# Kernel optimization log

Measured on AMD Instinct MI355X. Metric: run time of the kernel, lower is better.

## Reference

```python
import jax, jax.numpy as jnp
import numpy as np

SAMPLE_RATE = 4096.0  # matches init_kwargs sample_rate
STATE_DIM = 64
LENGTH, CHANNELS = 8192, 512


def setup_inputs() -> dict:
    key = jax.random.key(0)
    kx, kc = jax.random.split(key)
    x = jax.random.normal(kx, (LENGTH, CHANNELS), dtype=jnp.float32)
    # param init exactly as in the flax module
    logA = jnp.log(1.0 + jnp.arange(STATE_DIM, dtype=jnp.float32))
    B = jnp.ones((STATE_DIM,), dtype=jnp.float32)
    C = 0.01 * jax.random.normal(kc, (STATE_DIM,), dtype=jnp.float32)  # nn.initializers.normal() stddev=0.01
    return {"x": x, "logA": logA, "B": B, "C": C}


def reference(x, logA, B, C):
    # ZOH-style discretization: A = -exp(logA); Abar = exp(A*dt); Bbar = (Abar-1)*B/A
    dt = 1.0 / SAMPLE_RATE
    A = -jnp.exp(logA)                # (N,)
    Abar = jnp.exp(A * dt)            # (N,)
    Bbar = (Abar - 1.0) * B / A       # (N,)

    channels = x.shape[1]
    h0 = jnp.zeros((channels, logA.shape[0]), dtype=x.dtype)  # (C, N)

    def step(h, xt):
        # h: (C, N), xt: (C,)
        h = Abar[None, :] * h + xt[:, None] * Bbar[None, :]
        y = h @ C                      # (C,)
        return h, y

    _, y = jax.lax.scan(step, h0, x)   # y: (L, C)
    return y
```

## Files before the change

kernel.cpp:

```cpp
#include <hip/hip_runtime.h>
#include <math.h>

#define LENGTH   8192
#define CHANNELS 512
#define NSTATE   64
#define TCHUNK   64
#define NCHUNK   (LENGTH / TCHUNK)
#define E_ELEMS  (NCHUNK * NSTATE * CHANNELS)


__global__ void k_setup(const float* __restrict__ logA, const float* __restrict__ B,
                        const float* __restrict__ C, float* __restrict__ cons,
                        float* __restrict__ Gt, float* __restrict__ Tt,
                        float* __restrict__ Pt) {
    __shared__ double contrib[64][65];
    __shared__ double Kd[64];
    int n = threadIdx.x;

    double A    = -exp((double)logA[n]);
    double ab   = exp(A * (1.0 / 4096.0));
    double Bbar = (ab - 1.0) * (double)B[n] / A;
    double CB   = (double)C[n] * Bbar;

    cons[n]       = (float)ab;
    cons[64 + n]  = (float)CB;
    cons[128 + n] = (float)exp(A * (64.0 / 4096.0));

    double p = 1.0;
    #pragma unroll 1
    for (int e = 0; e < 64; ++e) { Gt[(63 - e) * 64 + n] = (float)p; p *= ab; }

    p = ab;
    #pragma unroll 1
    for (int t = 0; t < 64; ++t) { Pt[n * 64 + t] = (float)(CB * p); p *= ab; }

    p = CB;
    #pragma unroll 1
    for (int d = 0; d < 64; ++d) { contrib[n][d] = p; p *= ab; }
    __syncthreads();

    double Ksum = 0.0;
    #pragma unroll 1
    for (int m = 0; m < 64; ++m) Ksum += contrib[m][n];
    Kd[n] = Ksum;
    __syncthreads();

    int s = n;
    #pragma unroll 1
    for (int t = 0; t < 64; ++t) Tt[s * 64 + t] = (t >= s) ? (float)Kd[t - s] : 0.f;
}

__global__ __launch_bounds__(256, 4) void k_pass1(const float* __restrict__ x,
                                                  const float* __restrict__ Gt,
                                                  float* __restrict__ E) {
    __shared__ float Xl[64 * 64];
    int tid = threadIdx.x;
    int k   = blockIdx.x >> 3;
    int c0  = (blockIdx.x & 7) * 64;

    const float* xsrc = x + (size_t)k * TCHUNK * CHANNELS + c0;
    #pragma unroll
    for (int i = 0; i < 4; ++i) {
        int idx = tid + 256 * i;
        int s   = idx >> 4;
        int cq  = (idx & 15) * 4;
        *(float4*)&Xl[s * 64 + cq] = *(const float4*)(xsrc + (size_t)s * CHANNELS + cq);
    }
    __syncthreads();

    int w    = __builtin_amdgcn_readfirstlane(tid >> 6);
    int lane = tid & 63;
    const float* Gw = Gt + 16 * w;

    float acc[16];
    #pragma unroll
    for (int j = 0; j < 16; ++j) acc[j] = 0.f;

    #pragma unroll 4
    for (int s = 0; s < 64; ++s) {
        float xv = Xl[s * 64 + lane];
        const float* g = Gw + s * 64;
        #pragma unroll
        for (int j = 0; j < 16; ++j) acc[j] = fmaf(g[j], xv, acc[j]);
    }

    float* Ep = E + ((size_t)k * NSTATE + 16 * w) * CHANNELS + c0 + lane;
    #pragma unroll
    for (int j = 0; j < 16; ++j) Ep[(size_t)j * CHANNELS] = acc[j];
}

#define G2 16
__global__ __launch_bounds__(64, 1) void k_pass2(float* __restrict__ W,
                                                 const float* __restrict__ cons) {
    int gtid = blockIdx.x * 64 + threadIdx.x;
    int c = gtid & (CHANNELS - 1);
    int n = gtid >> 9;
    float aT = cons[128 + n];
    float* p = W + (size_t)n * CHANNELS + c;
    const size_t S = (size_t)NSTATE * CHANNELS;

    float e[2][G2];
    #pragma unroll
    for (int j = 0; j < G2; ++j) e[0][j] = p[(size_t)j * S];

    float hc = 0.f;
    #pragma unroll
    for (int k0 = 0; k0 < NCHUNK; k0 += G2) {
        const int cur = (k0 / G2) & 1;
        const int nxt = cur ^ 1;
        if (k0 + G2 < NCHUNK) {
            #pragma unroll
            for (int j = 0; j < G2; ++j) e[nxt][j] = p[(size_t)(k0 + G2 + j) * S];
        }
        #pragma unroll
        for (int j = 0; j < G2; ++j) {
            p[(size_t)(k0 + j) * S] = hc;
            hc = fmaf(aT, hc, e[cur][j]);
        }
    }
}

__global__ __launch_bounds__(256, 4) void k_pass3(const float* __restrict__ x,
                                                  const float* __restrict__ Tt,
                                                  const float* __restrict__ Pt,
                                                  const float* __restrict__ Wc,
                                                  float* __restrict__ y) {
    __shared__ float Xl[64 * 64];
    __shared__ float Hl[64 * 64];
    int tid = threadIdx.x;
    int k   = blockIdx.x >> 3;
    int c0  = (blockIdx.x & 7) * 64;

    const float* xsrc = x  + (size_t)k * TCHUNK * CHANNELS + c0;
    const float* hsrc = Wc + (size_t)k * NSTATE * CHANNELS + c0;
    #pragma unroll
    for (int i = 0; i < 4; ++i) {
        int idx = tid + 256 * i;
        int s   = idx >> 4;
        int cq  = (idx & 15) * 4;
        *(float4*)&Xl[s * 64 + cq] = *(const float4*)(xsrc + (size_t)s * CHANNELS + cq);
        *(float4*)&Hl[s * 64 + cq] = *(const float4*)(hsrc + (size_t)s * CHANNELS + cq);
    }
    __syncthreads();

    int w    = __builtin_amdgcn_readfirstlane(tid >> 6);
    int lane = tid & 63;
    int t0   = 16 * w;

    float acc[16];
    #pragma unroll
    for (int j = 0; j < 16; ++j) acc[j] = 0.f;

    const float* Tw = Tt + t0;
    #pragma unroll 4
    for (int s = 0; s < 64; ++s) {
        float xv = Xl[s * 64 + lane];
        const float* tt = Tw + s * 64;
        #pragma unroll
        for (int j = 0; j < 16; ++j) acc[j] = fmaf(tt[j], xv, acc[j]);
    }

    const float* Pw = Pt + t0;
    #pragma unroll 4
    for (int n = 0; n < 64; ++n) {
        float hv = Hl[n * 64 + lane];
        const float* pp = Pw + n * 64;
        #pragma unroll
        for (int j = 0; j < 16; ++j) acc[j] = fmaf(pp[j], hv, acc[j]);
    }

    float* yp = y + ((size_t)k * TCHUNK + t0) * CHANNELS + c0 + lane;
    #pragma unroll
    for (int j = 0; j < 16; ++j) yp[(size_t)j * CHANNELS] = acc[j];
}

__global__ __launch_bounds__(256) void k_fallback(const float* __restrict__ x,
                                                  const float* __restrict__ logA,
                                                  const float* __restrict__ B,
                                                  const float* __restrict__ C,
                                                  float* __restrict__ y) {
    int c = blockIdx.x * blockDim.x + threadIdx.x;
    if (c >= CHANNELS) return;
    float Abar[NSTATE], CB[NSTATE], h[NSTATE];
    for (int n = 0; n < NSTATE; ++n) {
        double A    = -exp((double)logA[n]);
        double ab   = exp(A * (1.0 / 4096.0));
        double Bbar = (ab - 1.0) * (double)B[n] / A;
        Abar[n] = (float)ab;
        CB[n]   = (float)((double)C[n] * Bbar);
        h[n]    = 0.f;
    }
    for (int t = 0; t < LENGTH; ++t) {
        float xv = x[(size_t)t * CHANNELS + c];
        float acc = 0.f;
        for (int n = 0; n < NSTATE; ++n) {
            h[n] = fmaf(Abar[n], h[n], xv);
            acc  = fmaf(CB[n], h[n], acc);
        }
        y[(size_t)t * CHANNELS + c] = acc;
    }
}

extern "C" void kernel_launch(void* const* d_in, const int* in_sizes, int n_in,
                              void* d_out, int out_size, void* d_ws, size_t ws_size,
                              hipStream_t stream) {
    const float* x    = (const float*)d_in[0];
    const float* logA = (const float*)d_in[1];
    const float* B    = (const float*)d_in[2];
    const float* C    = (const float*)d_in[3];
    float* yout = (float*)d_out;

    size_t need = (size_t)(E_ELEMS + 192 + 3 * 4096) * sizeof(float);
    if (ws_size < need) {
        k_fallback<<<(CHANNELS + 255) / 256, 256, 0, stream>>>(x, logA, B, C, yout);
        return;
    }

    float* W    = (float*)d_ws;
    float* cons = W + E_ELEMS;
    float* Gt   = cons + 192;
    float* Tt   = Gt + 4096;
    float* Pt   = Tt + 4096;

    k_setup<<<1, 64, 0, stream>>>(logA, B, C, cons, Gt, Tt, Pt);
    k_pass1<<<NCHUNK * 8, 256, 0, stream>>>(x, Gt, W);
    k_pass2<<<(NSTATE * CHANNELS) / 64, 64, 0, stream>>>(W, cons);
    k_pass3<<<NCHUNK * 8, 256, 0, stream>>>(x, Tt, Pt, W, yout);
}
```

Baseline: 113.9 us.

## Fold setup kernel into passes and use 4x4 register-tiled LDS matmuls

Removes the single-block double-precision setup kernel and instead recomputes the decay powers, Toeplitz kernel and output projection tables in shared memory inside each pass block using fp32 exp2f. The inner products in pass1 and pass3 change from per-lane scalar loops reading tables from global memory to a 4x4 register tile that reads float4 operands from LDS. This removes one serial launch and its double-precision latency, at the cost of redundant per-block table construction, more LDS use (lower occupancy bound in pass3) and reduced precision in the coefficients.

```diff
diff --git a/kernel.cpp b/kernel.cpp
--- a/kernel.cpp
+++ b/kernel.cpp
@@ -7,95 +7,74 @@
 #define TCHUNK   64
 #define NCHUNK   (LENGTH / TCHUNK)
 #define E_ELEMS  (NCHUNK * NSTATE * CHANNELS)
-
-
-__global__ void k_setup(const float* __restrict__ logA, const float* __restrict__ B,
-                        const float* __restrict__ C, float* __restrict__ cons,
-                        float* __restrict__ Gt, float* __restrict__ Tt,
-                        float* __restrict__ Pt) {
-    __shared__ double contrib[64][65];
-    __shared__ double Kd[64];
-    int n = threadIdx.x;
-
-    double A    = -exp((double)logA[n]);
-    double ab   = exp(A * (1.0 / 4096.0));
-    double Bbar = (ab - 1.0) * (double)B[n] / A;
-    double CB   = (double)C[n] * Bbar;
-
-    cons[n]       = (float)ab;
-    cons[64 + n]  = (float)CB;
-    cons[128 + n] = (float)exp(A * (64.0 / 4096.0));
-
-    double p = 1.0;
-    #pragma unroll 1
-    for (int e = 0; e < 64; ++e) { Gt[(63 - e) * 64 + n] = (float)p; p *= ab; }
-
-    p = ab;
-    #pragma unroll 1
-    for (int t = 0; t < 64; ++t) { Pt[n * 64 + t] = (float)(CB * p); p *= ab; }
-
-    p = CB;
-    #pragma unroll 1
-    for (int d = 0; d < 64; ++d) { contrib[n][d] = p; p *= ab; }
-    __syncthreads();
-
-    double Ksum = 0.0;
-    #pragma unroll 1
-    for (int m = 0; m < 64; ++m) Ksum += contrib[m][n];
-    Kd[n] = Ksum;
-    __syncthreads();
-
-    int s = n;
-    #pragma unroll 1
-    for (int t = 0; t < 64; ++t) Tt[s * 64 + t] = (t >= s) ? (float)Kd[t - s] : 0.f;
-}
+#define LOG2E    1.4426950408889634f
+#define DT       (1.0f / 4096.0f)
+
 
 __global__ __launch_bounds__(256, 4) void k_pass1(const float* __restrict__ x,
-                                                  const float* __restrict__ Gt,
+                                                  const float* __restrict__ logA,
                                                   float* __restrict__ E) {
     __shared__ float Xl[64 * 64];
+    __shared__ float Gl[64 * 64];
+    __shared__ float l2ab[64];
     int tid = threadIdx.x;
     int k   = blockIdx.x >> 3;
-    int c0  = (blockIdx.x & 7) * 64;
-
-    const float* xsrc = x + (size_t)k * TCHUNK * CHANNELS + c0;
+    int c0g = (blockIdx.x & 7) * 64;
+
+    if (tid < 64) {
+        float A = -expf(logA[tid]);
+        l2ab[tid] = A * DT * LOG2E;
+    }
+    const float* xsrc = x + (size_t)k * TCHUNK * CHANNELS + c0g;
     #pragma unroll
     for (int i = 0; i < 4; ++i) {
         int idx = tid + 256 * i;
-        int s   = idx >> 4;
-        int cq  = (idx & 15) * 4;
+        int s = idx >> 4, cq = (idx & 15) * 4;
         *(float4*)&Xl[s * 64 + cq] = *(const float4*)(xsrc + (size_t)s * CHANNELS + cq);
     }
     __syncthreads();
-
-    int w    = __builtin_amdgcn_readfirstlane(tid >> 6);
-    int lane = tid & 63;
-    const float* Gw = Gt + 16 * w;
-
-    float acc[16];
-    #pragma unroll
-    for (int j = 0; j < 16; ++j) acc[j] = 0.f;
-
-    #pragma unroll 4
+    {
+        int s = tid >> 2, nb = (tid & 3) * 16;
+        float e = (float)(63 - s);
+        #pragma unroll
+        for (int j = 0; j < 16; ++j) Gl[s * 64 + nb + j] = exp2f(e * l2ab[nb + j]);
+    }
+    __syncthreads();
+
+    int c0 = (tid & 15) * 4;
+    int n0 = (tid >> 4) * 4;
+    float a00=0,a01=0,a02=0,a03=0, a10=0,a11=0,a12=0,a13=0;
+    float a20=0,a21=0,a22=0,a23=0, a30=0,a31=0,a32=0,a33=0;
+
+    #pragma unroll 8
     for (int s = 0; s < 64; ++s) {
-        float xv = Xl[s * 64 + lane];
-        const float* g = Gw + s * 64;
-        #pragma unroll
-        for (int j = 0; j < 16; ++j) acc[j] = fmaf(g[j], xv, acc[j]);
-    }
-
-    float* Ep = E + ((size_t)k * NSTATE + 16 * w) * CHANNELS + c0 + lane;
-    #pragma unroll
-    for (int j = 0; j < 16; ++j) Ep[(size_t)j * CHANNELS] = acc[j];
+        float4 xv = *(const float4*)&Xl[s * 64 + c0];
+        float4 gv = *(const float4*)&Gl[s * 64 + n0];
+        a00 = fmaf(gv.x, xv.x, a00); a01 = fmaf(gv.x, xv.y, a01);
+        a02 = fmaf(gv.x, xv.z, a02); a03 = fmaf(gv.x, xv.w, a03);
+        a10 = fmaf(gv.y, xv.x, a10); a11 = fmaf(gv.y, xv.y, a11);
+        a12 = fmaf(gv.y, xv.z, a12); a13 = fmaf(gv.y, xv.w, a13);
+        a20 = fmaf(gv.z, xv.x, a20); a21 = fmaf(gv.z, xv.y, a21);
+        a22 = fmaf(gv.z, xv.z, a22); a23 = fmaf(gv.z, xv.w, a23);
+        a30 = fmaf(gv.w, xv.x, a30); a31 = fmaf(gv.w, xv.y, a31);
+        a32 = fmaf(gv.w, xv.z, a32); a33 = fmaf(gv.w, xv.w, a33);
+    }
+
+    float* Ep = E + ((size_t)k * NSTATE + n0) * CHANNELS + c0g + c0;
+    *(float4*)(Ep)                    = make_float4(a00, a01, a02, a03);
+    *(float4*)(Ep + 1 * CHANNELS)     = make_float4(a10, a11, a12, a13);
+    *(float4*)(Ep + 2 * CHANNELS)     = make_float4(a20, a21, a22, a23);
+    *(float4*)(Ep + 3 * CHANNELS)     = make_float4(a30, a31, a32, a33);
 }
 
 #define G2 16
 __global__ __launch_bounds__(64, 1) void k_pass2(float* __restrict__ W,
-                                                 const float* __restrict__ cons) {
+                                                 const float* __restrict__ logA) {
     int gtid = blockIdx.x * 64 + threadIdx.x;
     int c = gtid & (CHANNELS - 1);
     int n = gtid >> 9;
-    float aT = cons[128 + n];
+    float A  = -expf(logA[n]);
+    float aT = exp2f(A * (64.0f * DT) * LOG2E);
     float* p = W + (size_t)n * CHANNELS + c;
     const size_t S = (size_t)NSTATE * CHANNELS;
 
@@ -120,58 +99,106 @@
     }
 }
 
-__global__ __launch_bounds__(256, 4) void k_pass3(const float* __restrict__ x,
-                                                  const float* __restrict__ Tt,
-                                                  const float* __restrict__ Pt,
+__global__ __launch_bounds__(256, 2) void k_pass3(const float* __restrict__ x,
+                                                  const float* __restrict__ logA,
+                                                  const float* __restrict__ Bv,
+                                                  const float* __restrict__ Cv,
                                                   const float* __restrict__ Wc,
                                                   float* __restrict__ y) {
     __shared__ float Xl[64 * 64];
     __shared__ float Hl[64 * 64];
+    __shared__ float Tl[64 * 64];
+    __shared__ float Pl[64 * 64];
+    __shared__ float l2ab[64], CBl[64], Kl[64], Kpart[4 * 64];
     int tid = threadIdx.x;
     int k   = blockIdx.x >> 3;
-    int c0  = (blockIdx.x & 7) * 64;
-
-    const float* xsrc = x  + (size_t)k * TCHUNK * CHANNELS + c0;
-    const float* hsrc = Wc + (size_t)k * NSTATE * CHANNELS + c0;
+    int c0g = (blockIdx.x & 7) * 64;
+
+    if (tid < 64) {
+        int n = tid;
+        float A    = -expf(logA[n]);
+        float Bbar = expm1f(A * DT) * Bv[n] / A;
+        l2ab[n] = A * DT * LOG2E;
+        CBl[n]  = Cv[n] * Bbar;
+    }
+    const float* xsrc = x  + (size_t)k * TCHUNK * CHANNELS + c0g;
+    const float* hsrc = Wc + (size_t)k * NSTATE * CHANNELS + c0g;
     #pragma unroll
     for (int i = 0; i < 4; ++i) {
         int idx = tid + 256 * i;
-        int s   = idx >> 4;
-        int cq  = (idx & 15) * 4;
+        int s = idx >> 4, cq = (idx & 15) * 4;
         *(float4*)&Xl[s * 64 + cq] = *(const float4*)(xsrc + (size_t)s * CHANNELS + cq);
         *(float4*)&Hl[s * 64 + cq] = *(const float4*)(hsrc + (size_t)s * CHANNELS + cq);
     }
     __syncthreads();
-
-    int w    = __builtin_amdgcn_readfirstlane(tid >> 6);
-    int lane = tid & 63;
-    int t0   = 16 * w;
-
-    float acc[16];
-    #pragma unroll
-    for (int j = 0; j < 16; ++j) acc[j] = 0.f;
-
-    const float* Tw = Tt + t0;
+    {
+        int n = tid >> 2, tb = (tid & 3) * 16;
+        float l2 = l2ab[n], cb = CBl[n];
+        #pragma unroll
+        for (int j = 0; j < 16; ++j)
+            Pl[n * 64 + tb + j] = cb * exp2f((float)(tb + j + 1) * l2);
+    }
+    {
+        int d = tid & 63, q = tid >> 6;
+        float s = 0.f;
+        #pragma unroll
+        for (int i = 0; i < 16; ++i) {
+            int n = q * 16 + i;
+            s = fmaf(CBl[n], exp2f((float)d * l2ab[n]), s);
+        }
+        Kpart[q * 64 + d] = s;
+    }
+    __syncthreads();
+    if (tid < 64)
+        Kl[tid] = (Kpart[tid] + Kpart[64 + tid]) + (Kpart[128 + tid] + Kpart[192 + tid]);
+    __syncthreads();
+    {
+        int s = tid >> 2, tb = (tid & 3) * 16;
+        #pragma unroll
+        for (int j = 0; j < 16; ++j) {
+            int t = tb + j;
+            Tl[s * 64 + t] = (t >= s) ? Kl[t - s] : 0.f;
+        }
+    }
+    __syncthreads();
+
+    int c0 = (tid & 15) * 4;
+    int t0 = (tid >> 4) * 4;
+    float a00=0,a01=0,a02=0,a03=0, a10=0,a11=0,a12=0,a13=0;
+    float a20=0,a21=0,a22=0,a23=0, a30=0,a31=0,a32=0,a33=0;
+
     #pragma unroll 4
     for (int s = 0; s < 64; ++s) {
-        float xv = Xl[s * 64 + lane];
-        const float* tt = Tw + s * 64;
-        #pragma unroll
-        for (int j = 0; j < 16; ++j) acc[j] = fmaf(tt[j], xv, acc[j]);
-    }
-
-    const float* Pw = Pt + t0;
+        float4 xv = *(const float4*)&Xl[s * 64 + c0];
+        float4 tv = *(const float4*)&Tl[s * 64 + t0];
+        a00 = fmaf(tv.x, xv.x, a00); a01 = fmaf(tv.x, xv.y, a01);
+        a02 = fmaf(tv.x, xv.z, a02); a03 = fmaf(tv.x, xv.w, a03);
+        a10 = fmaf(tv.y, xv.x, a10); a11 = fmaf(tv.y, xv.y, a11);
+        a12 = fmaf(tv.y, xv.z, a12); a13 = fmaf(tv.y, xv.w, a13);
+        a20 = fmaf(tv.z, xv.x, a20); a21 = fmaf(tv.z, xv.y, a21);
+        a22 = fmaf(tv.z, xv.z, a22); a23 = fmaf(tv.z, xv.w, a23);
+        a30 = fmaf(tv.w, xv.x, a30); a31 = fmaf(tv.w, xv.y, a31);
+        a32 = fmaf(tv.w, xv.z, a32); a33 = fmaf(tv.w, xv.w, a33);
+    }
     #pragma unroll 4
     for (int n = 0; n < 64; ++n) {
-        float hv = Hl[n * 64 + lane];
-        const float* pp = Pw + n * 64;
-        #pragma unroll
-        for (int j = 0; j < 16; ++j) acc[j] = fmaf(pp[j], hv, acc[j]);
-    }
-
-    float* yp = y + ((size_t)k * TCHUNK + t0) * CHANNELS + c0 + lane;
-    #pragma unroll
-    for (int j = 0; j < 16; ++j) yp[(size_t)j * CHANNELS] = acc[j];
+        float4 hv = *(const float4*)&Hl[n * 64 + c0];
+        float4 pv = *(const float4*)&Pl[n * 64 + t0];
+        a00 = fmaf(pv.x, hv.x, a00); a01 = fmaf(pv.x, hv.y, a01);
+        a02 = fmaf(pv.x, hv.z, a02); a03 = fmaf(pv.x, hv.w, a03);
+        a10 = fmaf(pv.y, hv.x, a10); a11 = fmaf(pv.y, hv.y, a11);
+        a12 = fmaf(pv.y, hv.z, a12); a13 = fmaf(pv.y, hv.w, a13);
+        a20 = fmaf(pv.z, hv.x, a20); a21 = fmaf(pv.z, hv.y, a21);
+        a22 = fmaf(pv.z, hv.z, a22); a23 = fmaf(pv.z, hv.w, a23);
+        a30 = fmaf(pv.w, hv.x, a30); a31 = fmaf(pv.w, hv.y, a31);
+        a32 = fmaf(pv.w, hv.z, a32); a33 = fmaf(pv.w, hv.w, a33);
+    }
+
+    float* yp = y + ((size_t)k * TCHUNK + t0) * CHANNELS + c0g + c0;
+    *(float4*)(yp)                = make_float4(a00, a01, a02, a03);
+    *(float4*)(yp + 1 * CHANNELS) = make_float4(a10, a11, a12, a13);
+    *(float4*)(yp + 2 * CHANNELS) = make_float4(a20, a21, a22, a23);
+    *(float4*)(yp + 3 * CHANNELS) = make_float4(a30, a31, a32, a33);
 }
 
 __global__ __launch_bounds__(256) void k_fallback(const float* __restrict__ x,
@@ -183,11 +210,11 @@
     if (c >= CHANNELS) return;
     float Abar[NSTATE], CB[NSTATE], h[NSTATE];
     for (int n = 0; n < NSTATE; ++n) {
-        double A    = -exp((double)logA[n]);
-        double ab   = exp(A * (1.0 / 4096.0));
-        double Bbar = (ab - 1.0) * (double)B[n] / A;
-        Abar[n] = (float)ab;
-        CB[n]   = (float)((double)C[n] * Bbar);
+        float A    = -expf(logA[n]);
+        float ab   = exp2f(A * DT * LOG2E);
+        float Bbar = expm1f(A * DT) * B[n] / A;
+        Abar[n] = ab;
+        CB[n]   = C[n] * Bbar;
         h[n]    = 0.f;
     }
     for (int t = 0; t < LENGTH; ++t) {
@@ -210,20 +237,13 @@
     const float* C    = (const float*)d_in[3];
     float* yout = (float*)d_out;
 
-    size_t need = (size_t)(E_ELEMS + 192 + 3 * 4096) * sizeof(float);
-    if (ws_size < need) {
+    if (ws_size < (size_t)E_ELEMS * sizeof(float)) {
         k_fallback<<<(CHANNELS + 255) / 256, 256, 0, stream>>>(x, logA, B, C, yout);
         return;
     }
-
-    float* W    = (float*)d_ws;
-    float* cons = W + E_ELEMS;
-    float* Gt   = cons + 192;
-    float* Tt   = Gt + 4096;
-    float* Pt   = Tt + 4096;
-
-    k_setup<<<1, 64, 0, stream>>>(logA, B, C, cons, Gt, Tt, Pt);
-    k_pass1<<<NCHUNK * 8, 256, 0, stream>>>(x, Gt, W);
-    k_pass2<<<(NSTATE * CHANNELS) / 64, 64, 0, stream>>>(W, cons);
-    k_pass3<<<NCHUNK * 8, 256, 0, stream>>>(x, Tt, Pt, W, yout);
-}
+    float* W = (float*)d_ws;
+
+    k_pass1<<<NCHUNK * 8, 256, 0, stream>>>(x, logA, W);
+    k_pass2<<<(NSTATE * CHANNELS) / 64, 64, 0, stream>>>(W, logA);
+    k_pass3<<<NCHUNK * 8, 256, 0, stream>>>(x, logA, B, C, W, yout);
+}
```

After: 109.1 us, median of 2. 4.2% less time.
